# Optimization experiments

Measured on AMD Instinct MI355X. Metric: run time of the kernel, lower is better.

## Reference

```python
import jax, jax.numpy as jnp
import numpy as np

LR, HR, H, D1 = 512, 2048, 4, 200
N = 2 * HR            # 4096 nodes (fully connected graph)
C1 = D1 // H          # 50  per-head dim, layer 1
C2 = HR // H          # 512 per-head dim, layer 2
EPS = 1e-5


def setup_inputs() -> dict:
    key = jax.random.key(0)
    ks = jax.random.split(key, 24)
    lin = lambda k, fi, fo: jax.random.normal(k, (fi, fo), jnp.float32) * 0.02
    vec = lambda k, d: jax.random.normal(k, (d,), jnp.float32) * 0.02
    inp = {"lr_x": jax.random.normal(ks[0], (LR, N), jnp.float32)}
    # TransformerConv 1: lr -> 200 (query/key/value/skip linears, each with bias)
    inp["Wq1"], inp["bq1"] = lin(ks[1], LR, D1), vec(ks[2], D1)
    inp["Wk1"], inp["bk1"] = lin(ks[3], LR, D1), vec(ks[4], D1)
    inp["Wv1"], inp["bv1"] = lin(ks[5], LR, D1), vec(ks[6], D1)
    inp["Ws1"], inp["bs1"] = lin(ks[7], LR, D1), vec(ks[8], D1)
    # GraphNorm 1
    inp["gn1_w"] = 1.0 + 0.1 * jax.random.normal(ks[9], (D1,), jnp.float32)
    inp["gn1_b"] = vec(ks[10], D1)
    inp["gn1_ms"] = 1.0 + 0.1 * jax.random.normal(ks[11], (D1,), jnp.float32)
    # TransformerConv 2: 200 -> 2048
    inp["Wq2"], inp["bq2"] = lin(ks[12], D1, HR), vec(ks[13], HR)
    inp["Wk2"], inp["bk2"] = lin(ks[14], D1, HR), vec(ks[15], HR)
    inp["Wv2"], inp["bv2"] = lin(ks[16], D1, HR), vec(ks[17], HR)
    inp["Ws2"], inp["bs2"] = lin(ks[18], D1, HR), vec(ks[19], HR)
    # GraphNorm 2
    inp["gn2_w"] = 1.0 + 0.1 * jax.random.normal(ks[20], (HR,), jnp.float32)
    inp["gn2_b"] = vec(ks[21], HR)
    inp["gn2_ms"] = 1.0 + 0.1 * jax.random.normal(ks[22], (HR,), jnp.float32)
    return inp


def _transformer_conv(x, Wq, bq, Wk, bk, Wv, bv, Ws, bs, heads, ch):
    # PyG TransformerConv on a fully-connected edge_index == dense multi-head attention
    n = x.shape[0]
    q = (x @ Wq + bq).reshape(n, heads, ch)
    k = (x @ Wk + bk).reshape(n, heads, ch)
    v = (x @ Wv + bv).reshape(n, heads, ch)
    scores = jnp.einsum('ihc,jhc->hij', q, k) / (ch ** 0.5)  # [H, N, N]
    attn = jax.nn.softmax(scores, axis=-1)                   # softmax over source nodes j
    out = jnp.einsum('hij,jhc->ihc', attn, v).reshape(n, heads * ch)
    return out + x @ Ws + bs                                 # root/skip connection


def _graph_norm(x, w, b, ms):
    # PyG GraphNorm: y = w * (x - ms*mean) / sqrt(E[(x - ms*mean)^2] + eps) + b
    mean = jnp.mean(x, axis=0, keepdims=True)
    out = x - mean * ms
    var = jnp.mean(out * out, axis=0, keepdims=True)
    return out * jax.lax.rsqrt(var + EPS) * w + b


def reference(lr_x, Wq1, bq1, Wk1, bk1, Wv1, bv1, Ws1, bs1, gn1_w, gn1_b, gn1_ms,
              Wq2, bq2, Wk2, bk2, Wv2, bv2, Ws2, bs2, gn2_w, gn2_b, gn2_ms):
    h = _transformer_conv(lr_x.T, Wq1, bq1, Wk1, bk1, Wv1, bv1, Ws1, bs1, H, C1)  # [N, 200]
    h = _graph_norm(h, gn1_w, gn1_b, gn1_ms)
    h2 = _transformer_conv(h, Wq2, bq2, Wk2, bk2, Wv2, bv2, Ws2, bs2, H, C2)      # [N, HR]
    h2 = _graph_norm(h2, gn2_w, gn2_b, gn2_ms).T                                  # [HR, N]
    h2 = h2 / jnp.linalg.norm(h2, axis=1, keepdims=True)
    return jax.nn.relu(h2 @ h2.T)                                                 # [HR, HR]
```

## Files before the change

### kernel.cpp

```cpp
#include <hip/hip_runtime.h>
#include <math.h>

typedef unsigned int u32;
typedef unsigned short ushort_t;
typedef __attribute__((ext_vector_type(8))) short short8;
typedef __attribute__((ext_vector_type(4))) float f32x4;

__device__ __forceinline__ ushort_t f2bf(float x) {
  u32 u = __float_as_uint(x);
  u32 r = (u + 0x7fffu + ((u >> 16) & 1u)) >> 16;
  return (ushort_t)r;
}
__device__ __forceinline__ float bf2f(u32 s) {
  return __uint_as_float(s << 16);
}
__device__ __forceinline__ void ld4bf(const ushort_t* p, float* o) {
  uint2 u = *(const uint2*)p;
  o[0] = bf2f(u.x & 0xffffu); o[1] = bf2f(u.x >> 16);
  o[2] = bf2f(u.y & 0xffffu); o[3] = bf2f(u.y >> 16);
}

__device__ __forceinline__ float block_sum256(float v, float* red) {
  #pragma unroll
  for (int o = 32; o > 0; o >>= 1) v += __shfl_down(v, o, 64);
  __syncthreads();
  if ((threadIdx.x & 63) == 0) red[threadIdx.x >> 6] = v;
  __syncthreads();
  return red[0] + red[1] + red[2] + red[3];
}

__global__ __launch_bounds__(512) void fused_attn1(
    const ushort_t* __restrict__ qk, const ushort_t* __restrict__ v,
    float* __restrict__ oP, float* __restrict__ r1p, float scale)
{
  __shared__ ushort_t Kl[2][4096];
  __shared__ ushort_t Vl[2][4096];
  __shared__ ushort_t Pl[128][80];
  const int t = threadIdx.x;
  const int lane = t & 63;
  const int wv = t >> 6;
  const int h = blockIdx.y;
  const int m0 = blockIdx.x * 128;
  const int z = blockIdx.z;
  const int lr = lane & 15;
  const int hk = lane >> 4;

  short8 aq0, aq1;
  {
    const ushort_t* qrow = qk + (size_t)(m0 + wv * 16 + lr) * 512 + h * 64;
    aq0 = *(const short8*)(qrow + hk * 8);
    aq1 = *(const short8*)(qrow + 32 + hk * 8);
  }

  f32x4 oAcc[4];
  #pragma unroll
  for (int i = 0; i < 4; ++i) oAcc[i] = (f32x4){0.f, 0.f, 0.f, 0.f};
  float racc[4] = {0.f, 0.f, 0.f, 0.f};

  const size_t kbase = (size_t)256 + h * 64;
  const int rS = t >> 3;
  const int cS = t & 7;
  const int lcS = cS ^ (rS & 7);

  {
    const int n0 = z * 16 * 64;
    __builtin_amdgcn_global_load_lds(
        (const __attribute__((address_space(1))) u32*)(qk + (size_t)(n0 + rS) * 512 + kbase + lcS * 8),
        (__attribute__((address_space(3))) u32*)(&Kl[0][t * 8]), 16, 0, 0);
    __builtin_amdgcn_global_load_lds(
        (const __attribute__((address_space(1))) u32*)(v + (size_t)(h * 128 + rS) * 4096 + n0 + lcS * 8),
        (__attribute__((address_space(3))) u32*)(&Vl[0][t * 8]), 16, 0, 0);
  }
  __syncthreads();

  int cur = 0;
  for (int it = 0; it < 16; ++it) {
    if (it + 1 < 16) {
      const int n1 = (z * 16 + it + 1) * 64;
      __builtin_amdgcn_global_load_lds(
          (const __attribute__((address_space(1))) u32*)(qk + (size_t)(n1 + rS) * 512 + kbase + lcS * 8),
          (__attribute__((address_space(3))) u32*)(&Kl[cur ^ 1][t * 8]), 16, 0, 0);
      __builtin_amdgcn_global_load_lds(
          (const __attribute__((address_space(1))) u32*)(v + (size_t)(h * 128 + rS) * 4096 + n1 + lcS * 8),
          (__attribute__((address_space(3))) u32*)(&Vl[cur ^ 1][t * 8]), 16, 0, 0);
    }
    f32x4 sA[4];
    #pragma unroll
    for (int nf = 0; nf < 4; ++nf) {
      const int rl = nf * 16 + lr;
      const char* kb = (const char*)&Kl[cur][0] + rl * 128;
      short8 b0 = *(const short8*)(kb + ((hk ^ (rl & 7)) * 16));
      short8 b1 = *(const short8*)(kb + (((4 + hk) ^ (rl & 7)) * 16));
      f32x4 sa = (f32x4){0.f, 0.f, 0.f, 0.f};
      sa = __builtin_amdgcn_mfma_f32_16x16x32_bf16(aq0, b0, sa, 0, 0, 0);
      sa = __builtin_amdgcn_mfma_f32_16x16x32_bf16(aq1, b1, sa, 0, 0, 0);
      sA[nf] = sa;
    }
    #pragma unroll
    for (int nf = 0; nf < 4; ++nf) {
      #pragma unroll
      for (int r = 0; r < 4; ++r) {
        float e = exp2f(sA[nf][r] * scale);
        racc[r] += e;
        Pl[wv * 16 + hk * 4 + r][nf * 16 + lr] = f2bf(e);
      }
    }
    short8 ap0 = *(const short8*)&Pl[wv * 16 + lr][hk * 8];
    short8 ap1 = *(const short8*)&Pl[wv * 16 + lr][32 + hk * 8];
    #pragma unroll
    for (int ff = 0; ff < 4; ++ff) {
      const int rl = ff * 16 + lr;
      const char* vb = (const char*)&Vl[cur][0] + rl * 128;
      short8 b0 = *(const short8*)(vb + ((hk ^ (rl & 7)) * 16));
      short8 b1 = *(const short8*)(vb + (((4 + hk) ^ (rl & 7)) * 16));
      oAcc[ff] = __builtin_amdgcn_mfma_f32_16x16x32_bf16(ap0, b0, oAcc[ff], 0, 0, 0);
      oAcc[ff] = __builtin_amdgcn_mfma_f32_16x16x32_bf16(ap1, b1, oAcc[ff], 0, 0, 0);
    }
    __syncthreads();
    cur ^= 1;
  }

  #pragma unroll
  for (int r = 0; r < 4; ++r) {
    racc[r] += __shfl_xor(racc[r], 1);
    racc[r] += __shfl_xor(racc[r], 2);
    racc[r] += __shfl_xor(racc[r], 4);
    racc[r] += __shfl_xor(racc[r], 8);
  }
  if (lr == 0) {
    float* rp = r1p + ((size_t)z * 4 + h) * 4096;
    #pragma unroll
    for (int r = 0; r < 4; ++r) rp[m0 + wv * 16 + hk * 4 + r] = racc[r];
  }
  float* ob = oP + (size_t)z * 512 * 4096;
  #pragma unroll
  for (int ff = 0; ff < 4; ++ff) {
    const size_t fbase = (size_t)(h * 128 + ff * 16 + lr) * 4096;
    #pragma unroll
    for (int r = 0; r < 4; ++r) {
      const int q = m0 + wv * 16 + hk * 4 + r;
      ob[fbase + q] = oAcc[ff][r];
    }
  }
}

__global__ __launch_bounds__(512) void fused_attn2(
    const ushort_t* __restrict__ Tm, const ushort_t* __restrict__ X,
    const ushort_t* __restrict__ Xt, float* __restrict__ Up, float scale)
{
  __shared__ ushort_t Xl[2][16384];
  __shared__ ushort_t Xtl[2][16384];
  __shared__ ushort_t Pl[128][68];
  const int t = threadIdx.x;
  const int lane = t & 63;
  const int wv = t >> 6;
  const int h = blockIdx.y;
  const int m0 = blockIdx.x * 128;
  const int z = blockIdx.z;
  const int lr = lane & 15;
  const int hk = lane >> 4;

  short8 tq[8];
  {
    const ushort_t* trow = Tm + ((size_t)h * 4096 + m0 + wv * 16 + lr) * 256;
    #pragma unroll
    for (int s = 0; s < 8; ++s) tq[s] = *(const short8*)(trow + s * 32 + hk * 8);
  }

  f32x4 uAcc[16];
  #pragma unroll
  for (int i = 0; i < 16; ++i) uAcc[i] = (f32x4){0.f, 0.f, 0.f, 0.f};

  auto stage = [&](int buf, int n0) {
    #pragma unroll
    for (int i = 0; i < 4; ++i) {
      const int st = t + i * 512;
      const int row = st >> 5, ph = st & 31;
      const int lc = (ph & 24) | ((ph & 7) ^ (row & 7));
      __builtin_amdgcn_global_load_lds(
          (const __attribute__((address_space(1))) u32*)(X + (size_t)(n0 + row) * 256 + lc * 8),
          (__attribute__((address_space(3))) u32*)(&Xl[buf][st * 8]), 16, 0, 0);
    }
    #pragma unroll
    for (int i = 0; i < 4; ++i) {
      const int st = t + i * 512;
      const int row = st >> 3, ph = st & 7;
      const int lc = ph ^ (row & 7);
      __builtin_amdgcn_global_load_lds(
          (const __attribute__((address_space(1))) u32*)(Xt + (size_t)row * 4096 + n0 + lc * 8),
          (__attribute__((address_space(3))) u32*)(&Xtl[buf][st * 8]), 16, 0, 0);
    }
  };

  stage(0, z * 2048);
  __syncthreads();

  int cur = 0;
  for (int it = 0; it < 32; ++it) {
    if (it + 1 < 32) stage(cur ^ 1, z * 2048 + (it + 1) * 64);
    const char* xb = (const char*)&Xl[cur][0];
    #pragma unroll
    for (int nf = 0; nf < 4; ++nf) {
      const int row = nf * 16 + lr;
      const char* rb = xb + row * 512;
      f32x4 sa = (f32x4){0.f, 0.f, 0.f, 0.f};
      #pragma unroll
      for (int s = 0; s < 8; ++s) {
        const int c = s * 4 + hk;
        const int ph = (c & 24) | ((c & 7) ^ (row & 7));
        short8 xf = *(const short8*)(rb + ph * 16);
        sa = __builtin_amdgcn_mfma_f32_16x16x32_bf16(xf, tq[s], sa, 0, 0, 0);
      }
      #pragma unroll
      for (int r = 0; r < 4; ++r)
        Pl[wv * 16 + lr][nf * 16 + hk * 4 + r] = f2bf(exp2f(sa[r] * scale));
    }
    short8 ap0 = *(const short8*)((const char*)&Pl[wv * 16 + lr][0] + hk * 16);
    short8 ap1 = *(const short8*)((const char*)&Pl[wv * 16 + lr][0] + (4 + hk) * 16);
    const char* xtb = (const char*)&Xtl[cur][0];
    #pragma unroll
    for (int ff = 0; ff < 16; ++ff) {
      const int row = ff * 16 + lr;
      const char* rb2 = xtb + row * 128;
      short8 x0 = *(const short8*)(rb2 + ((hk ^ (row & 7)) * 16));
      short8 x1 = *(const short8*)(rb2 + (((4 + hk) ^ (row & 7)) * 16));
      uAcc[ff] = __builtin_amdgcn_mfma_f32_16x16x32_bf16(x0, ap0, uAcc[ff], 0, 0, 0);
      uAcc[ff] = __builtin_amdgcn_mfma_f32_16x16x32_bf16(x1, ap1, uAcc[ff], 0, 0, 0);
    }
    __syncthreads();
    cur ^= 1;
  }

  float* ub = Up + ((size_t)(z * 4 + h) * 256) * 4096;
  #pragma unroll
  for (int ff = 0; ff < 16; ++ff) {
    #pragma unroll
    for (int r = 0; r < 4; ++r) {
      const int a = ff * 16 + hk * 4 + r;
      ub[(size_t)a * 4096 + m0 + wv * 16 + lr] = uAcc[ff][r];
    }
  }
}

__global__ __launch_bounds__(256) void combine_u(
    const float* __restrict__ Up, ushort_t* __restrict__ Usum,
    float* __restrict__ r2)
{
  __shared__ float tl[64][65];
  const int t = threadIdx.x;
  const int qt = blockIdx.x;
  const int at = blockIdx.y;
  const int h  = blockIdx.z;
  const int c = t & 63;
  const int rb = t >> 6;
  #pragma unroll
  for (int i = 0; i < 16; ++i) {
    const int r = rb + i * 4;
    const int a = at * 64 + r;
    const int q = qt * 64 + c;
    const size_t i0 = ((size_t)h * 256 + a) * 4096 + q;
    float val = Up[i0] + Up[(size_t)4 * 256 * 4096 + i0];
    tl[r][c] = val;
    if (a == 200) r2[(size_t)h * 4096 + q] = val;
  }
  __syncthreads();
  #pragma unroll
  for (int i = 0; i < 16; ++i) {
    const int r = rb + i * 4;
    const int q = qt * 64 + r;
    const int a = at * 64 + c;
    Usum[((size_t)h * 4096 + q) * 256 + a] = f2bf(tl[c][r]);
  }
}

#define RD_A(bb, mm, cc) (*(const short8*)(lsAc + (bb)*32768 + arow + (mm)*2048 + (cc)))
#define RD_B(bb, nn, cc) (*(const short8*)(lsBc + (bb)*32768 + brow + (nn)*2048 + (cc)))

#define MM8(nn, bv) { \
  acc[0][nn] = __builtin_amdgcn_mfma_f32_16x16x32_bf16(a0, bv, acc[0][nn], 0,0,0); \
  acc[1][nn] = __builtin_amdgcn_mfma_f32_16x16x32_bf16(a1, bv, acc[1][nn], 0,0,0); \
  acc[2][nn] = __builtin_amdgcn_mfma_f32_16x16x32_bf16(a2, bv, acc[2][nn], 0,0,0); \
  acc[3][nn] = __builtin_amdgcn_mfma_f32_16x16x32_bf16(a3, bv, acc[3][nn], 0,0,0); \
  acc[4][nn] = __builtin_amdgcn_mfma_f32_16x16x32_bf16(a4, bv, acc[4][nn], 0,0,0); \
  acc[5][nn] = __builtin_amdgcn_mfma_f32_16x16x32_bf16(a5, bv, acc[5][nn], 0,0,0); \
  acc[6][nn] = __builtin_amdgcn_mfma_f32_16x16x32_bf16(a6, bv, acc[6][nn], 0,0,0); \
  acc[7][nn] = __builtin_amdgcn_mfma_f32_16x16x32_bf16(a7, bv, acc[7][nn], 0,0,0); }

#define STG(BASE, LD, LS, bb, hf, tt) { \
  _Pragma("unroll") \
  for (int ii = 0; ii < 2; ++ii) { \
    const int s_ = t + ii * 512; \
    const int r_ = s_ >> 3; \
    const int lc_ = (s_ & 7) ^ (r_ & 7); \
    __builtin_amdgcn_global_load_lds( \
      (const __attribute__((address_space(1))) u32*)((BASE) + (size_t)((hf) * 128 + r_) * (LD) + (size_t)(tt) * 64 + lc_ * 8), \
      (__attribute__((address_space(3))) u32*)(&(LS)[bb][(hf) * 8192 + s_ * 8]), 16, 0, 0); \
  } }

#define BAR() __builtin_amdgcn_s_barrier()
#define PRIO(x) __builtin_amdgcn_s_setprio(x)

#define GRP(bf, tS1, tS2) { \
  a0=RD_A(bf,0,c0); a1=RD_A(bf,1,c0); a2=RD_A(bf,2,c0); a3=RD_A(bf,3,c0); \
  a4=RD_A(bf,4,c0); a5=RD_A(bf,5,c0); a6=RD_A(bf,6,c0); a7=RD_A(bf,7,c0); \
  b0=RD_B(bf,0,c0); b1=RD_B(bf,1,c0); \
  STG(Ab, lda, lsA, 1-(bf), 1, tS1); STG(Bb, ldb, lsB, 1-(bf), 0, tS1); \
  BAR(); PRIO(1); MM8(0, b0); MM8(1, b1); PRIO(0); BAR(); \
  b2=RD_B(bf,2,c0); b3=RD_B(bf,3,c0); \
  STG(Bb, ldb, lsB, 1-(bf), 1, tS1); \
  BAR(); PRIO(1); MM8(2, b2); MM8(3, b3); PRIO(0); BAR(); \
  a0=RD_A(bf,0,c1); a1=RD_A(bf,1,c1); a2=RD_A(bf,2,c1); a3=RD_A(bf,3,c1); \
  a4=RD_A(bf,4,c1); a5=RD_A(bf,5,c1); a6=RD_A(bf,6,c1); a7=RD_A(bf,7,c1); \
  b0=RD_B(bf,0,c1); b1=RD_B(bf,1,c1); \
  BAR(); PRIO(1); MM8(0, b0); MM8(1, b1); PRIO(0); BAR(); \
  b2=RD_B(bf,2,c1); b3=RD_B(bf,3,c1); \
  STG(Ab, lda, lsA, (bf), 0, tS2); \
  BAR(); PRIO(1); MM8(2, b2); MM8(3, b3); PRIO(0); \
  asm volatile("s_waitcnt vmcnt(2)" ::: "memory"); \
  BAR(); }

template<int CMODE, bool RELU>
__global__ __launch_bounds__(512, 2) void mfma256_8ph(
    const ushort_t* __restrict__ A, const ushort_t* __restrict__ B,
    void* __restrict__ Cv, int lda, int ldb, int ldc,
    int K, int zsplit, size_t zA, size_t zB, size_t zC,
    int bShift, size_t bHead, int Mvalid, float scale)
{
  __shared__ ushort_t lsA[2][16384];
  __shared__ ushort_t lsB[2][16384];
  const int t = threadIdx.x;
  const int gx = gridDim.x;
  const int nwg = gx * gridDim.y;
  const int bid = blockIdx.y * gx + blockIdx.x;
  const int qq = nwg >> 3, rr_ = nwg & 7;
  const int xcd = bid & 7, idx = bid >> 3;
  const int swz = (xcd < rr_ ? xcd * (qq + 1) : rr_ * (qq + 1) + (xcd - rr_) * qq) + idx;
  const int m0 = (swz / gx) * 256;
  const int n0 = (swz % gx) * 256;
  const int z = blockIdx.z;
  int Kc = K, kOff = 0;
  size_t aZ = 0, bZ = 0, cZ = 0;
  if (zsplit > 1) { Kc = K / zsplit; kOff = z * Kc; cZ = (size_t)z * zC; }
  else { aZ = (size_t)z * zA; bZ = (size_t)z * zB; cZ = (size_t)z * zC; }
  const ushort_t* Ab = A + aZ + (size_t)m0 * lda + kOff;
  const ushort_t* Bb = B + bZ + (size_t)n0 * ldb + kOff
                     + (bShift >= 0 ? (size_t)(m0 >> bShift) * bHead : 0);
  const int NT = Kc / 64;

  f32x4 acc[8][4];
  #pragma unroll
  for (int i = 0; i < 8; ++i)
    #pragma unroll
    for (int j = 0; j < 4; ++j) acc[i][j] = (f32x4){0.f, 0.f, 0.f, 0.f};

  const int lane = t & 63;
  const int wv = t >> 6;
  const int wr = (wv >> 2) * 128;
  const int wc = (wv & 3) * 64;
  const int lr = lane & 15;
  const int kc = lane >> 4;
  const int sw = lane & 7;
  const int c0 = (kc ^ sw) * 16;
  const int c1 = c0 ^ 64;
  const int arow = (wr + lr) * 128;
  const int brow = (wc + lr) * 128;
  const char* lsAc = (const char*)lsA;
  const char* lsBc = (const char*)lsB;

  short8 a0, a1, a2, a3, a4, a5, a6, a7, b0, b1, b2, b3;

  STG(Ab, lda, lsA, 0, 0, 0); STG(Ab, lda, lsA, 0, 1, 0);
  STG(Bb, ldb, lsB, 0, 0, 0); STG(Bb, ldb, lsB, 0, 1, 0);
  STG(Ab, lda, lsA, 1, 0, 1);
  asm volatile("s_waitcnt vmcnt(2)" ::: "memory");
  BAR();

  const int NITER = NT >> 1;
  for (int it = 0; it < NITER; ++it) {
    const int tb = 2 * it;
    const int s1 = tb + 1;
    const int s2 = (tb + 2 < NT) ? tb + 2 : 0;
    const int s3 = (tb + 3 < NT) ? tb + 3 : 0;
    GRP(0, s1, s2)
    GRP(1, s2, s3)
  }

  const int row4 = (lane >> 4) * 4;
  const int coln = lane & 15;
  float* Cf = (float*)Cv + cZ;
  ushort_t* Ch = (ushort_t*)Cv + cZ;
  #pragma unroll
  for (int m = 0; m < 8; ++m) {
    #pragma unroll
    for (int r = 0; r < 4; ++r) {
      const int gm = m0 + wr + m * 16 + row4 + r;
      const bool ok = gm < Mvalid;
      #pragma unroll
      for (int n = 0; n < 4; ++n) {
        const int gn = n0 + wc + n * 16 + coln;
        float v = acc[m][n][r] * scale;
        if (RELU) v = fmaxf(v, 0.f);
        if (ok) {
          if (CMODE == 0)      Cf[(size_t)gm * ldc + gn] = v;
          else if (CMODE == 1) Ch[(size_t)gm * ldc + gn] = f2bf(v);
          else                 atomicAdd(&Cf[(size_t)gm * ldc + gn], v);
        }
      }
    }
  }
}

#undef GRP
#undef STG
#undef MM8
#undef RD_A
#undef RD_B

template<int CMODE, bool RELU>
__global__ __launch_bounds__(256) void mfma_bt(
    const ushort_t* __restrict__ A, const ushort_t* __restrict__ B,
    void* __restrict__ Cv, int lda, int ldb, int ldc,
    int K, int Ksplit, size_t zA, size_t zB, size_t zC,
    int bShift, size_t bHead, int mMask, int Mvalid, float scale)
{
  __shared__ ushort_t lsA[2][128 * 32];
  __shared__ ushort_t lsB[2][128 * 32];
  const int t  = threadIdx.x;
  const int m0 = blockIdx.y * 128;
  const int n0 = blockIdx.x * 128;
  const int z = blockIdx.z;
  int Kc = K, kOff = 0;
  size_t aZ = 0, bZ = 0, cZ = 0;
  if (Ksplit > 1) { Kc = K / Ksplit; kOff = z * Kc; cZ = (size_t)z * zC; }
  else { aZ = (size_t)z * zA; bZ = (size_t)z * zB; cZ = (size_t)z * zC; }
  const int NT = Kc / 32;
  const ushort_t* Ab = A + aZ + (size_t)m0 * lda + kOff;
  const ushort_t* Bb = B + bZ + (size_t)n0 * ldb + kOff
                     + (bShift >= 0 ? (size_t)(m0 >> bShift) * bHead : 0);
  const int cs = t & 3;

  f32x4 acc[4][4];
  #pragma unroll
  for (int i = 0; i < 4; ++i)
    #pragma unroll
    for (int j = 0; j < 4; ++j) acc[i][j] = (f32x4){0.f, 0.f, 0.f, 0.f};

  const int lane = t & 63;
  const int wv = t >> 6;
  const int wr = (wv >> 1) * 64;
  const int wc = (wv & 1) * 64;
  const int lr = lane & 15;
  const int kc = lane >> 4;

  int roffA[4], roffB[4];
  #pragma unroll
  for (int m = 0; m < 4; ++m) {
    int ra = wr + m * 16 + lr;
    roffA[m] = ra * 64 + ((kc ^ (ra & 3)) * 16);
    int rb = wc + m * 16 + lr;
    roffB[m] = rb * 64 + ((kc ^ (rb & 3)) * 16);
  }

  auto stage = [&](int buf, int kt) {
    const ushort_t* As = Ab + kt * 32;
    const ushort_t* Bs = Bb + kt * 32;
    #pragma unroll
    for (int i = 0; i < 2; ++i) {
      int s = t + i * 256;
      int r = s >> 2;
      int c = cs ^ (r & 3);
      __builtin_amdgcn_global_load_lds(
          (const __attribute__((address_space(1))) u32*)(As + (size_t)r * lda + c * 8),
          (__attribute__((address_space(3))) u32*)(&lsA[buf][s * 8]), 16, 0, 0);
    }
    #pragma unroll
    for (int i = 0; i < 2; ++i) {
      int s = t + i * 256;
      int r = s >> 2;
      int c = cs ^ (r & 3);
      __builtin_amdgcn_global_load_lds(
          (const __attribute__((address_space(1))) u32*)(Bs + (size_t)r * ldb + c * 8),
          (__attribute__((address_space(3))) u32*)(&lsB[buf][s * 8]), 16, 0, 0);
    }
  };

  stage(0, 0);
  __syncthreads();
  int cur = 0;
  for (int kt = 0; kt < NT; ++kt) {
    if (kt + 1 < NT) stage(cur ^ 1, kt + 1);
    short8 af[4], bfr[4];
    const char* baseA = (const char*)&lsA[cur][0];
    const char* baseB = (const char*)&lsB[cur][0];
    #pragma unroll
    for (int m = 0; m < 4; ++m) af[m]  = *(const short8*)(baseA + roffA[m]);
    #pragma unroll
    for (int n = 0; n < 4; ++n) bfr[n] = *(const short8*)(baseB + roffB[n]);
    #pragma unroll
    for (int m = 0; m < 4; ++m)
      #pragma unroll
      for (int n = 0; n < 4; ++n)
        acc[m][n] = __builtin_amdgcn_mfma_f32_16x16x32_bf16(af[m], bfr[n], acc[m][n], 0, 0, 0);
    __syncthreads();
    cur ^= 1;
  }

  const int row4 = (lane >> 4) * 4;
  const int coln = lane & 15;
  float* Cf = (float*)Cv + cZ;
  ushort_t* Ch = (ushort_t*)Cv + cZ;
  #pragma unroll
  for (int m = 0; m < 4; ++m) {
    #pragma unroll
    for (int r = 0; r < 4; ++r) {
      const int gm = m0 + wr + m * 16 + row4 + r;
      const bool ok = (mMask >= 0) ? ((gm & mMask) < Mvalid) : (gm < Mvalid);
      #pragma unroll
      for (int n = 0; n < 4; ++n) {
        const int gn = n0 + wc + n * 16 + coln;
        float v = acc[m][n][r] * scale;
        if (RELU) v = fmaxf(v, 0.f);
        if (ok) {
          if (CMODE == 0)      Cf[(size_t)gm * ldc + gn] = v;
          else if (CMODE == 1) Ch[(size_t)gm * ldc + gn] = f2bf(v);
          else                 atomicAdd(&Cf[(size_t)gm * ldc + gn], v);
        }
      }
    }
  }
}

__global__ __launch_bounds__(256) void wt_conv(
    const float* __restrict__ W, const float* __restrict__ bias,
    ushort_t* __restrict__ dst, int Mtot, int ldw, int Kv, int Kp,
    int PADH, int VALH)
{
  const int m = blockIdx.x;
  const int h = m / PADH, c0 = m % PADH;
  const int fout = h * VALH + c0;
  const bool valid = (c0 < VALH) && (fout < Mtot);
  for (int k = threadIdx.x; k < Kp; k += blockDim.x) {
    float v = 0.f;
    if (valid) {
      if (k < Kv) v = W[(size_t)k * ldw + fout];
      else if (k == Kv) v = bias[fout];
    }
    dst[(size_t)m * Kp + k] = f2bf(v);
  }
}

__global__ __launch_bounds__(256) void wt_trans(
    const float* __restrict__ W, const float* __restrict__ bias,
    ushort_t* __restrict__ dst)
{
  const int rid = blockIdx.x;
  const int h = rid >> 8, a = rid & 255;
  for (int f = threadIdx.x; f < 512; f += 256) {
    float v = 0.f;
    if (a < 200)       v = W[(size_t)a * 2048 + h * 512 + f];
    else if (a == 200) v = bias[h * 512 + f];
    dst[(size_t)rid * 512 + f] = f2bf(v);
  }
}

__global__ __launch_bounds__(256) void xt_conv(
    const float* __restrict__ h1nT, ushort_t* __restrict__ Xt)
{
  const int a = blockIdx.x;
  for (int q = threadIdx.x; q < 4096; q += 256) {
    float v = (a < 200) ? h1nT[(size_t)a * 4096 + q] : ((a == 200) ? 1.f : 0.f);
    Xt[(size_t)a * 4096 + q] = f2bf(v);
  }
}

__global__ __launch_bounds__(256) void trans_pad(
    const float* __restrict__ src, ushort_t* __restrict__ dst, int Kv, int Kp)
{
  __shared__ float tl[64][65];
  const int t = threadIdx.x;
  const int f0 = blockIdx.x * 64;
  const int i0 = blockIdx.y * 64;
  const int c = t & 63, rbase = t >> 6;
  #pragma unroll
  for (int it = 0; it < 16; ++it) {
    int r = rbase + it * 4;
    int f = f0 + r;
    tl[r][c] = (f < Kv) ? src[(size_t)f * 4096 + i0 + c] : 0.f;
  }
  __syncthreads();
  #pragma unroll
  for (int it = 0; it < 16; ++it) {
    int r = rbase + it * 4;
    int f = f0 + c;
    if (f < Kp) {
      float v = (f < Kv) ? tl[c][r] : ((f == Kv) ? 1.f : 0.f);
      dst[(size_t)(i0 + r) * Kp + f] = f2bf(v);
    }
  }
}

__global__ __launch_bounds__(256) void graph_norm_attn1(
    const float* __restrict__ skip, const float* __restrict__ oP,
    const float* __restrict__ r1p, float* __restrict__ out,
    const float* __restrict__ w, const float* __restrict__ b,
    const float* __restrict__ ms)
{
  __shared__ float red[4];
  const int t = threadIdx.x;
  const int row = blockIdx.x;
  const int h = row / 50;
  const int pr = h * 128 + row % 50;
  const float* sk = skip + (size_t)pr * 4096;
  const size_t OSTR = (size_t)512 * 4096;
  float v[16];
  float s = 0.f;
  #pragma unroll
  for (int e = 0; e < 4; ++e) {
    const int idx = t * 4 + 1024 * e;
    float4 a = *(const float4*)&sk[idx];
    float4 o0 = *(const float4*)&oP[(size_t)pr * 4096 + idx];
    float4 o1 = *(const float4*)&oP[OSTR + (size_t)pr * 4096 + idx];
    float4 o2 = *(const float4*)&oP[2 * OSTR + (size_t)pr * 4096 + idx];
    float4 o3 = *(const float4*)&oP[3 * OSTR + (size_t)pr * 4096 + idx];
    float4 r0 = *(const float4*)&r1p[(size_t)h * 4096 + idx];
    float4 r1 = *(const float4*)&r1p[(size_t)(4 + h) * 4096 + idx];
    float4 r2 = *(const float4*)&r1p[(size_t)(8 + h) * 4096 + idx];
    float4 r3 = *(const float4*)&r1p[(size_t)(12 + h) * 4096 + idx];
    v[e*4+0] = a.x + (o0.x + o1.x + o2.x + o3.x) / (r0.x + r1.x + r2.x + r3.x);
    v[e*4+1] = a.y + (o0.y + o1.y + o2.y + o3.y) / (r0.y + r1.y + r2.y + r3.y);
    v[e*4+2] = a.z + (o0.z + o1.z + o2.z + o3.z) / (r0.z + r1.z + r2.z + r3.z);
    v[e*4+3] = a.w + (o0.w + o1.w + o2.w + o3.w) / (r0.w + r1.w + r2.w + r3.w);
    s += v[e*4+0] + v[e*4+1] + v[e*4+2] + v[e*4+3];
  }
  const float mean = block_sum256(s, red) * (1.f / 4096.f);
  const float sub = mean * ms[row];
  float s2 = 0.f;
  #pragma unroll
  for (int e = 0; e < 16; ++e) { v[e] -= sub; s2 += v[e] * v[e]; }
  const float var = block_sum256(s2, red) * (1.f / 4096.f);
  const float scl = rsqrtf(var + 1e-5f) * w[row];
  const float bb = b[row];
  float* y = out + (size_t)row * 4096;
  #pragma unroll
  for (int e = 0; e < 4; ++e) {
    float o0[4];
    #pragma unroll
    for (int q = 0; q < 4; ++q) o0[q] = v[e * 4 + q] * scl + bb;
    *(float4*)&y[t * 4 + 1024 * e] = *(float4*)&o0[0];
  }
}

__global__ __launch_bounds__(256) void graph_norm_attn2(
    const ushort_t* __restrict__ skip, const ushort_t* __restrict__ O,
    const float* __restrict__ r2, ushort_t* __restrict__ out,
    const float* __restrict__ w, const float* __restrict__ b,
    const float* __restrict__ ms)
{
  __shared__ float red[4];
  const int t = threadIdx.x;
  const int row = blockIdx.x;
  const ushort_t* sk = skip + (size_t)row * 4096;
  const ushort_t* pa = O + (size_t)row * 4096;
  const float* rr = r2 + (size_t)(row >> 9) * 4096;
  float v[16];
  float s = 0.f;
  #pragma unroll
  for (int e = 0; e < 4; ++e) {
    const int idx = t * 4 + 1024 * e;
    float a[4], oa[4];
    ld4bf(&sk[idx], a); ld4bf(&pa[idx], oa);
    float4 rv = *(const float4*)&rr[idx];
    v[e*4+0] = a[0] + oa[0] / rv.x;
    v[e*4+1] = a[1] + oa[1] / rv.y;
    v[e*4+2] = a[2] + oa[2] / rv.z;
    v[e*4+3] = a[3] + oa[3] / rv.w;
    s += v[e*4+0] + v[e*4+1] + v[e*4+2] + v[e*4+3];
  }
  const float mean = block_sum256(s, red) * (1.f / 4096.f);
  const float sub = mean * ms[row];
  float s2 = 0.f;
  #pragma unroll
  for (int e = 0; e < 16; ++e) { v[e] -= sub; s2 += v[e] * v[e]; }
  const float var = block_sum256(s2, red) * (1.f / 4096.f);
  const float scl = rsqrtf(var + 1e-5f) * w[row];
  const float bb = b[row];
  #pragma unroll
  for (int e = 0; e < 16; ++e) v[e] = v[e] * scl + bb;
  float s3 = 0.f;
  #pragma unroll
  for (int e = 0; e < 16; ++e) s3 += v[e] * v[e];
  const float osc = rsqrtf(block_sum256(s3, red));
  ushort_t* y = out + (size_t)row * 4096;
  #pragma unroll
  for (int e = 0; e < 4; ++e) {
    ushort_t o0[4];
    #pragma unroll
    for (int q = 0; q < 4; ++q) o0[q] = f2bf(v[e * 4 + q] * osc);
    *(ushort2*)&y[t * 4 + 1024 * e] = *(ushort2*)&o0[0];
    *(ushort2*)&y[t * 4 + 1024 * e + 2] = *(ushort2*)&o0[2];
  }
}

__global__ __launch_bounds__(256) void add4_relu_bf16(
    const ushort_t* __restrict__ g, float* __restrict__ out)
{
  const size_t i = (size_t)blockIdx.x * 256 + threadIdx.x;
  const size_t ss = (size_t)2048 * 2048;
  float a[4], b[4], c[4], d[4];
  ld4bf(&g[i * 4], a);
  ld4bf(&g[ss + i * 4], b);
  ld4bf(&g[2 * ss + i * 4], c);
  ld4bf(&g[3 * ss + i * 4], d);
  float4 o;
  o.x = fmaxf(a[0] + b[0] + c[0] + d[0], 0.f);
  o.y = fmaxf(a[1] + b[1] + c[1] + d[1], 0.f);
  o.z = fmaxf(a[2] + b[2] + c[2] + d[2], 0.f);
  o.w = fmaxf(a[3] + b[3] + c[3] + d[3], 0.f);
  ((float4*)out)[i] = o;
}

extern "C" void kernel_launch(void* const* d_in, const int* in_sizes, int n_in,
                              void* d_out, int out_size, void* d_ws, size_t ws_size,
                              hipStream_t stream)
{
  (void)in_sizes; (void)n_in; (void)out_size; (void)ws_size;
  const float* lr_x = (const float*)d_in[0];
  const float* Wq1 = (const float*)d_in[1];  const float* bq1 = (const float*)d_in[2];
  const float* Wk1 = (const float*)d_in[3];  const float* bk1 = (const float*)d_in[4];
  const float* Wv1 = (const float*)d_in[5];  const float* bv1 = (const float*)d_in[6];
  const float* Ws1 = (const float*)d_in[7];  const float* bs1 = (const float*)d_in[8];
  const float* gn1w = (const float*)d_in[9]; const float* gn1b = (const float*)d_in[10];
  const float* gn1ms = (const float*)d_in[11];
  const float* Wq2 = (const float*)d_in[12]; const float* bq2 = (const float*)d_in[13];
  const float* Wk2 = (const float*)d_in[14]; const float* bk2 = (const float*)d_in[15];
  const float* Wv2 = (const float*)d_in[16]; const float* bv2 = (const float*)d_in[17];
  const float* Ws2 = (const float*)d_in[18]; const float* bs2 = (const float*)d_in[19];
  const float* gn2w = (const float*)d_in[20]; const float* gn2b = (const float*)d_in[21];
  const float* gn2ms = (const float*)d_in[22];

  char* p = (char*)d_ws;
  auto alloc = [&](size_t bytes) { char* r = p; p += (bytes + 255) & ~(size_t)255; return r; };
  char*     scrA = alloc((size_t)32 * 1024 * 1024);
  ushort_t* xb   = (ushort_t*)alloc((size_t)4096 * 544 * 2);
  ushort_t* qk1b = (ushort_t*)alloc((size_t)4096 * 512 * 2);
  ushort_t* v1b  = (ushort_t*)alloc((size_t)512 * 4096 * 2);
  char*     u0   = alloc((size_t)16 * 1024 * 1024);
  float*    s1p  = (float*)u0;
  float*    h1nT = (float*)   alloc((size_t)200 * 4096 * 4);
  ushort_t* h1nb = (ushort_t*)alloc((size_t)4096 * 256 * 2);
  ushort_t* Wqk1 = (ushort_t*)alloc((size_t)512 * 544 * 2);
  ushort_t* Wv1b = (ushort_t*)alloc((size_t)512 * 544 * 2);
  ushort_t* Ws1p = (ushort_t*)alloc((size_t)512 * 544 * 2);
  ushort_t* Wcat = (ushort_t*)alloc((size_t)4096 * 256 * 2);
  ushort_t* Qt   = (ushort_t*)alloc((size_t)4 * 256 * 512 * 2);
  ushort_t* Kt   = (ushort_t*)alloc((size_t)4 * 256 * 512 * 2);
  ushort_t* Mtall= (ushort_t*)alloc((size_t)4 * 256 * 256 * 2);
  ushort_t* Tall = (ushort_t*)alloc((size_t)4 * 4096 * 256 * 2);
  ushort_t* Xtb  = (ushort_t*)alloc((size_t)256 * 4096 * 2);
  ushort_t* vs2b = (ushort_t*)alloc((size_t)4096 * 4096 * 2);
  ushort_t* Usum = (ushort_t*)alloc((size_t)4 * 4096 * 256 * 2);
  ushort_t* Opl  = (ushort_t*)alloc((size_t)2048 * 4096 * 2);
  float*    r1p  = (float*)   alloc((size_t)16 * 4096 * 4);
  float*    r2   = (float*)   alloc((size_t)4 * 4096 * 4);
  float*    oP   = (float*)scrA;
  float*    Up   = (float*)scrA;
  ushort_t* g4   = (ushort_t*)scrA;
  ushort_t* h2b  = (ushort_t*)u0;

  const dim3 b256(256, 1, 1);
  const dim3 b512(512, 1, 1);
  const float LOG2E = 1.4426950408889634f;
  const float sc1e = 0.14142135623730951f * LOG2E;
  const float sc2e = 0.04419417382415922f * LOG2E;

  wt_conv<<<dim3(256),  b256, 0, stream>>>(Wq1, bq1, Wqk1,             200, 200, 512, 544, 64, 50);
  wt_conv<<<dim3(256),  b256, 0, stream>>>(Wk1, bk1, Wqk1 + 256 * 544, 200, 200, 512, 544, 64, 50);
  wt_conv<<<dim3(512),  b256, 0, stream>>>(Wv1, bv1, Wv1b,             200, 200, 512, 544, 128, 50);
  wt_conv<<<dim3(512),  b256, 0, stream>>>(Ws1, bs1, Ws1p,             200, 200, 512, 544, 128, 50);
  wt_conv<<<dim3(2048), b256, 0, stream>>>(Wv2, bv2, Wcat,              2048, 2048, 200, 256, 2048, 2048);
  wt_conv<<<dim3(2048), b256, 0, stream>>>(Ws2, bs2, Wcat + 2048 * 256, 2048, 2048, 200, 256, 2048, 2048);
  wt_trans<<<dim3(1024), b256, 0, stream>>>(Wq2, bq2, Qt);
  wt_trans<<<dim3(1024), b256, 0, stream>>>(Wk2, bk2, Kt);
  trans_pad<<<dim3(9, 64), b256, 0, stream>>>(lr_x, xb, 512, 544);

  mfma_bt<1, false><<<dim3(4, 32), b256, 0, stream>>>(
      xb, Wqk1, qk1b, 544, 544, 512, 544, 1, 0, 0, 0, -1, 0, -1, 4096, 1.f);
  mfma_bt<1, false><<<dim3(32, 4), b256, 0, stream>>>(
      Wv1b, xb, v1b, 544, 544, 4096, 544, 1, 0, 0, 0, -1, 0, -1, 512, 1.f);
  mfma_bt<0, false><<<dim3(32, 4), b256, 0, stream>>>(
      Ws1p, xb, s1p, 544, 544, 4096, 544, 1, 0, 0, 0, -1, 0, 127, 50, 1.f);

  fused_attn1<<<dim3(32, 4, 4), b512, 0, stream>>>(qk1b, v1b, oP, r1p, sc1e);
  graph_norm_attn1<<<dim3(200), b256, 0, stream>>>(s1p, oP, r1p, h1nT, gn1w, gn1b, gn1ms);
  trans_pad<<<dim3(4, 64), b256, 0, stream>>>(h1nT, h1nb, 200, 256);
  xt_conv<<<dim3(256), b256, 0, stream>>>(h1nT, Xtb);

  mfma_bt<1, false><<<dim3(32, 32), b256, 0, stream>>>(
      Wcat, h1nb, vs2b, 256, 256, 4096, 256, 1, 0, 0, 0, -1, 0, -1, 4096, 1.f);

  mfma_bt<1, false><<<dim3(2, 2, 4), b256, 0, stream>>>(
      Kt, Qt, Mtall, 512, 512, 256, 512, 1,
      (size_t)256 * 512, (size_t)256 * 512, (size_t)256 * 256, -1, 0, -1, 256, 1.f);
  mfma_bt<1, false><<<dim3(2, 32, 4), b256, 0, stream>>>(
      h1nb, Mtall, Tall, 256, 256, 256, 256, 1,
      0, (size_t)256 * 256, (size_t)4096 * 256, -1, 0, -1, 4096, 1.f);
  fused_attn2<<<dim3(32, 4, 2), b512, 0, stream>>>(Tall, h1nb, Xtb, Up, sc2e);
  combine_u<<<dim3(64, 4, 4), b256, 0, stream>>>(Up, Usum, r2);
  mfma_bt<1, false><<<dim3(32, 16), b256, 0, stream>>>(
      Wcat, Usum, Opl, 256, 256, 4096, 256, 1,
      0, 0, 0, 9, (size_t)4096 * 256, -1, 2048, 1.f);
  graph_norm_attn2<<<dim3(2048), b256, 0, stream>>>(
      vs2b + (size_t)2048 * 4096, Opl, r2, h2b, gn2w, gn2b, gn2ms);

  mfma256_8ph<1, false><<<dim3(8, 8, 4), b512, 0, stream>>>(
      h2b, h2b, g4, 4096, 4096, 2048, 4096, 4,
      0, 0, (size_t)2048 * 2048, -1, 0, 2048, 1.f);
  add4_relu_bf16<<<dim3(4096), b256, 0, stream>>>(g4, (float*)d_out);
}
```

Measured before the change: 362.9 us.

## Double query tile per block in attn2, split keys four ways, store bf16 partials

fused_attn2 now handles 256 queries per block (32 per wave), so each staged key/value tile feeds twice as many MFMAs. The key range is split into four z-slices instead of two, with single-buffered X staging issued after the P write barrier. Partial U results are stored as bf16 instead of fp32 and combine_u sums four planes. This is meant to cut repeated loads of the shared key/value data and halve the traffic of the partial outputs. In exchange it adds an extra barrier per iteration, raises register pressure from the doubled accumulators, and loses some precision by rounding the partial sums to bf16.

```diff
diff --git a/kernel.cpp b/kernel.cpp
--- a/kernel.cpp
+++ b/kernel.cpp
@@ -144,34 +144,38 @@
   }
 }
 
-__global__ __launch_bounds__(512) void fused_attn2(
+__global__ __launch_bounds__(512, 2) void fused_attn2(
     const ushort_t* __restrict__ Tm, const ushort_t* __restrict__ X,
-    const ushort_t* __restrict__ Xt, float* __restrict__ Up, float scale)
-{
-  __shared__ ushort_t Xl[2][16384];
+    const ushort_t* __restrict__ Xt, ushort_t* __restrict__ Up, float scale)
+{
+  __shared__ ushort_t Xl[16384];
   __shared__ ushort_t Xtl[2][16384];
-  __shared__ ushort_t Pl[128][68];
+  __shared__ ushort_t Pl[256][66];
   const int t = threadIdx.x;
   const int lane = t & 63;
   const int wv = t >> 6;
   const int h = blockIdx.y;
-  const int m0 = blockIdx.x * 128;
+  const int m0 = blockIdx.x * 256;
   const int z = blockIdx.z;
   const int lr = lane & 15;
   const int hk = lane >> 4;
 
-  short8 tq[8];
-  {
-    const ushort_t* trow = Tm + ((size_t)h * 4096 + m0 + wv * 16 + lr) * 256;
-    #pragma unroll
-    for (int s = 0; s < 8; ++s) tq[s] = *(const short8*)(trow + s * 32 + hk * 8);
-  }
-
-  f32x4 uAcc[16];
-  #pragma unroll
-  for (int i = 0; i < 16; ++i) uAcc[i] = (f32x4){0.f, 0.f, 0.f, 0.f};
-
-  auto stage = [&](int buf, int n0) {
+  short8 tq[2][8];
+  #pragma unroll
+  for (int qb = 0; qb < 2; ++qb) {
+    const ushort_t* trow = Tm + ((size_t)h * 4096 + m0 + wv * 32 + qb * 16 + lr) * 256;
+    #pragma unroll
+    for (int s = 0; s < 8; ++s) tq[qb][s] = *(const short8*)(trow + s * 32 + hk * 8);
+  }
+
+  f32x4 uAcc[16][2];
+  #pragma unroll
+  for (int i = 0; i < 16; ++i) {
+    uAcc[i][0] = (f32x4){0.f, 0.f, 0.f, 0.f};
+    uAcc[i][1] = (f32x4){0.f, 0.f, 0.f, 0.f};
+  }
+
+  auto stageX = [&](int n0) {
     #pragma unroll
     for (int i = 0; i < 4; ++i) {
       const int st = t + i * 512;
@@ -179,8 +183,10 @@
       const int lc = (ph & 24) | ((ph & 7) ^ (row & 7));
       __builtin_amdgcn_global_load_lds(
           (const __attribute__((address_space(1))) u32*)(X + (size_t)(n0 + row) * 256 + lc * 8),
-          (__attribute__((address_space(3))) u32*)(&Xl[buf][st * 8]), 16, 0, 0);
-    }
+          (__attribute__((address_space(3))) u32*)(&Xl[st * 8]), 16, 0, 0);
+    }
+  };
+  auto stageXt = [&](int buf, int n0) {
     #pragma unroll
     for (int i = 0; i < 4; ++i) {
       const int st = t + i * 512;
@@ -192,31 +198,41 @@
     }
   };
 
-  stage(0, z * 2048);
+  const int base = z * 16;
+  stageX(base * 64);
+  stageXt(0, base * 64);
   __syncthreads();
 
   int cur = 0;
-  for (int it = 0; it < 32; ++it) {
-    if (it + 1 < 32) stage(cur ^ 1, z * 2048 + (it + 1) * 64);
-    const char* xb = (const char*)&Xl[cur][0];
+  for (int it = 0; it < 16; ++it) {
+    if (it + 1 < 16) stageXt(cur ^ 1, (base + it + 1) * 64);
+    const char* xb = (const char*)&Xl[0];
     #pragma unroll
     for (int nf = 0; nf < 4; ++nf) {
       const int row = nf * 16 + lr;
       const char* rb = xb + row * 512;
-      f32x4 sa = (f32x4){0.f, 0.f, 0.f, 0.f};
+      f32x4 sa0 = (f32x4){0.f, 0.f, 0.f, 0.f};
+      f32x4 sa1 = (f32x4){0.f, 0.f, 0.f, 0.f};
       #pragma unroll
       for (int s = 0; s < 8; ++s) {
         const int c = s * 4 + hk;
         const int ph = (c & 24) | ((c & 7) ^ (row & 7));
         short8 xf = *(const short8*)(rb + ph * 16);
-        sa = __builtin_amdgcn_mfma_f32_16x16x32_bf16(xf, tq[s], sa, 0, 0, 0);
+        sa0 = __builtin_amdgcn_mfma_f32_16x16x32_bf16(xf, tq[0][s], sa0, 0, 0, 0);
+        sa1 = __builtin_amdgcn_mfma_f32_16x16x32_bf16(xf, tq[1][s], sa1, 0, 0, 0);
       }
       #pragma unroll
-      for (int r = 0; r < 4; ++r)
-        Pl[wv * 16 + lr][nf * 16 + hk * 4 + r] = f2bf(exp2f(sa[r] * scale));
-    }
-    short8 ap0 = *(const short8*)((const char*)&Pl[wv * 16 + lr][0] + hk * 16);
-    short8 ap1 = *(const short8*)((const char*)&Pl[wv * 16 + lr][0] + (4 + hk) * 16);
+      for (int r = 0; r < 4; ++r) {
+        Pl[wv * 32 + lr][nf * 16 + hk * 4 + r]      = f2bf(exp2f(sa0[r] * scale));
+        Pl[wv * 32 + 16 + lr][nf * 16 + hk * 4 + r] = f2bf(exp2f(sa1[r] * scale));
+      }
+    }
+    __syncthreads();
+    if (it + 1 < 16) stageX((base + it + 1) * 64);
+    short8 p00 = *(const short8*)((const char*)&Pl[wv * 32 + lr][0] + hk * 16);
+    short8 p01 = *(const short8*)((const char*)&Pl[wv * 32 + lr][0] + (4 + hk) * 16);
+    short8 p10 = *(const short8*)((const char*)&Pl[wv * 32 + 16 + lr][0] + hk * 16);
+    short8 p11 = *(const short8*)((const char*)&Pl[wv * 32 + 16 + lr][0] + (4 + hk) * 16);
     const char* xtb = (const char*)&Xtl[cur][0];
     #pragma unroll
     for (int ff = 0; ff < 16; ++ff) {
@@ -224,26 +240,31 @@
       const char* rb2 = xtb + row * 128;
       short8 x0 = *(const short8*)(rb2 + ((hk ^ (row & 7)) * 16));
       short8 x1 = *(const short8*)(rb2 + (((4 + hk) ^ (row & 7)) * 16));
-      uAcc[ff] = __builtin_amdgcn_mfma_f32_16x16x32_bf16(x0, ap0, uAcc[ff], 0, 0, 0);
-      uAcc[ff] = __builtin_amdgcn_mfma_f32_16x16x32_bf16(x1, ap1, uAcc[ff], 0, 0, 0);
+      uAcc[ff][0] = __builtin_amdgcn_mfma_f32_16x16x32_bf16(x0, p00, uAcc[ff][0], 0, 0, 0);
+      uAcc[ff][0] = __builtin_amdgcn_mfma_f32_16x16x32_bf16(x1, p01, uAcc[ff][0], 0, 0, 0);
+      uAcc[ff][1] = __builtin_amdgcn_mfma_f32_16x16x32_bf16(x0, p10, uAcc[ff][1], 0, 0, 0);
+      uAcc[ff][1] = __builtin_amdgcn_mfma_f32_16x16x32_bf16(x1, p11, uAcc[ff][1], 0, 0, 0);
     }
     __syncthreads();
     cur ^= 1;
   }
 
-  float* ub = Up + ((size_t)(z * 4 + h) * 256) * 4096;
+  ushort_t* ub = Up + (size_t)(z * 4 + h) * 256 * 4096;
   #pragma unroll
   for (int ff = 0; ff < 16; ++ff) {
     #pragma unroll
-    for (int r = 0; r < 4; ++r) {
-      const int a = ff * 16 + hk * 4 + r;
-      ub[(size_t)a * 4096 + m0 + wv * 16 + lr] = uAcc[ff][r];
+    for (int qb = 0; qb < 2; ++qb) {
+      #pragma unroll
+      for (int r = 0; r < 4; ++r) {
+        const int a = ff * 16 + hk * 4 + r;
+        ub[(size_t)a * 4096 + m0 + wv * 32 + qb * 16 + lr] = f2bf(uAcc[ff][qb][r]);
+      }
     }
   }
 }
 
 __global__ __launch_bounds__(256) void combine_u(
-    const float* __restrict__ Up, ushort_t* __restrict__ Usum,
+    const ushort_t* __restrict__ Up, ushort_t* __restrict__ Usum,
     float* __restrict__ r2)
 {
   __shared__ float tl[64][65];
@@ -253,13 +274,15 @@
   const int h  = blockIdx.z;
   const int c = t & 63;
   const int rb = t >> 6;
+  const size_t PLN = (size_t)4 * 256 * 4096;
   #pragma unroll
   for (int i = 0; i < 16; ++i) {
     const int r = rb + i * 4;
     const int a = at * 64 + r;
     const int q = qt * 64 + c;
     const size_t i0 = ((size_t)h * 256 + a) * 4096 + q;
-    float val = Up[i0] + Up[(size_t)4 * 256 * 4096 + i0];
+    float val = bf2f(Up[i0]) + bf2f(Up[PLN + i0])
+              + bf2f(Up[2 * PLN + i0]) + bf2f(Up[3 * PLN + i0]);
     tl[r][c] = val;
     if (a == 200) r2[(size_t)h * 4096 + q] = val;
   }
@@ -763,7 +786,7 @@
   float*    r1p  = (float*)   alloc((size_t)16 * 4096 * 4);
   float*    r2   = (float*)   alloc((size_t)4 * 4096 * 4);
   float*    oP   = (float*)scrA;
-  float*    Up   = (float*)scrA;
+  ushort_t* UpH  = (ushort_t*)scrA;
   ushort_t* g4   = (ushort_t*)scrA;
   ushort_t* h2b  = (ushort_t*)u0;
 
@@ -804,8 +827,8 @@
   mfma_bt<1, false><<<dim3(2, 32, 4), b256, 0, stream>>>(
       h1nb, Mtall, Tall, 256, 256, 256, 256, 1,
       0, (size_t)256 * 256, (size_t)4096 * 256, -1, 0, -1, 4096, 1.f);
-  fused_attn2<<<dim3(32, 4, 2), b512, 0, stream>>>(Tall, h1nb, Xtb, Up, sc2e);
-  combine_u<<<dim3(64, 4, 4), b256, 0, stream>>>(Up, Usum, r2);
+  fused_attn2<<<dim3(16, 4, 4), b512, 0, stream>>>(Tall, h1nb, Xtb, UpH, sc2e);
+  combine_u<<<dim3(64, 4, 4), b256, 0, stream>>>(UpH, Usum, r2);
   mfma_bt<1, false><<<dim3(32, 16), b256, 0, stream>>>(
       Wcat, Usum, Opl, 256, 256, 4096, 256, 1,
       0, 0, 0, 9, (size_t)4096 * 256, -1, 2048, 1.f);
```

Measured after the change: 350.5 us. -3.4%, faster.
